# Kernel optimization log

Measured on AMD Instinct MI355X. Metric: run time of the kernel, lower is better.

Reference implementation:

```python
import jax, jax.numpy as jnp
import numpy as np

BLANK = 0
T, N, C, S = 1024, 64, 128, 128


def setup_inputs() -> dict:
    key = jax.random.key(0)
    k1, k2, k3, k4 = jax.random.split(key, 4)
    logits = jax.random.normal(k1, (T, N, C), dtype=jnp.float32)
    log_probs = jax.nn.log_softmax(logits, axis=-1)
    targets = jax.random.randint(k2, (N, S), 1, C).astype(jnp.int64)  # non-blank labels
    input_lengths = jax.random.randint(k3, (N,), T // 2, T + 1).astype(jnp.int32)
    target_lengths = jax.random.randint(k4, (N,), S // 2, S + 1).astype(jnp.int32)
    return {"log_probs": log_probs, "targets": targets,
            "input_lengths": input_lengths, "target_lengths": target_lengths}


def _ctc_loss(log_probs, targets, input_lengths, target_lengths):
    Tt, Nn, Cc = log_probs.shape
    Ss = targets.shape[1]
    Sx = 2 * Ss + 1  # extended target length (blanks interleaved)
    neg_inf = jnp.asarray(-jnp.inf, log_probs.dtype)

    ext = jnp.full((Nn, Sx), BLANK, dtype=jnp.int32).at[:, 1::2].set(targets.astype(jnp.int32))
    # emission log-prob of each extended state at each time: [T, N, Sx]
    emit = jnp.take_along_axis(log_probs, jnp.broadcast_to(ext[None], (Tt, Nn, Sx)), axis=2)
    # skip transition allowed when label[s] != label[s-2] (and s >= 2)
    skip = jnp.concatenate([jnp.zeros((Nn, 2), bool), ext[:, 2:] != ext[:, :-2]], axis=1)

    # faithful to the torch code: alphas initialized to ZEROS, then states 0,1 set
    alpha0 = jnp.zeros((Nn, Sx), log_probs.dtype)
    alpha0 = alpha0.at[:, 0].set(emit[0, :, 0]).at[:, 1].set(emit[0, :, 1])

    pad1 = jnp.full((Nn, 1), neg_inf, log_probs.dtype)
    pad2 = jnp.full((Nn, 2), neg_inf, log_probs.dtype)

    def step(alpha, emit_t):
        a_m1 = jnp.concatenate([pad1, alpha[:, :-1]], axis=1)
        a_m2 = jnp.where(skip, jnp.concatenate([pad2, alpha[:, :-2]], axis=1), neg_inf)
        new = jax.nn.logsumexp(jnp.stack([alpha, a_m1, a_m2]), axis=0) + emit_t
        return new, new

    _, rest = jax.lax.scan(step, alpha0, emit[1:])
    alphas = jnp.concatenate([alpha0[None], rest], axis=0)  # [T, N, Sx]

    n_idx = jnp.arange(Nn)
    v = alphas[input_lengths - 1, n_idx, 2 * target_lengths - 1]  # [N]
    # original: loss = -logsumexp over batch, then .mean() of a scalar (identity)
    return -jax.nn.logsumexp(v)


def reference(log_probs, targets, input_lengths, target_lengths):
    return _ctc_loss(log_probs, targets, input_lengths, target_lengths)
```

## Files before the change

### kernel.cpp

```cpp
#include <hip/hip_runtime.h>
#include <math.h>

#define TT 1024
#define NN 64
#define CC 128
#define SS 128
#define CH 32
#define NCHUNK 32
#define NC (NN * CC)

typedef float f4 __attribute__((ext_vector_type(4)));

#define DPP_QP_XOR1   0xB1
#define DPP_QP_XOR2   0x4E
#define DPP_WAVE_SHR1 0x138
#define DPP_ROW_MIRR  0x140
#define DPP_HALF_MIRR 0x141
#define DPP_BCAST15   0x142
#define DPP_BCAST31   0x143

template <int CTRL>
__device__ __forceinline__ float dpp_max_stage(float v) {
    int p = __builtin_amdgcn_update_dpp(__float_as_int(v), __float_as_int(v),
                                        CTRL, 0xF, 0xF, false);
    return fmaxf(v, __int_as_float(p));
}
__device__ __forceinline__ float dpp_shr1(float v) {
    int p = __builtin_amdgcn_update_dpp(0, __float_as_int(v),
                                        DPP_WAVE_SHR1, 0xF, 0xF, true);
    return __int_as_float(p);
}

#define DSR(dst, addr, off) \
    asm volatile("ds_read_b128 %0, %1 offset:" #off : "=v"(dst) : "v"(addr))
#define LGKM(n) do { \
    asm volatile("s_waitcnt lgkmcnt(" #n ")" ::: "memory"); \
    __builtin_amdgcn_sched_barrier(0); } while (0)
#define VMC(n) do { \
    asm volatile("s_waitcnt vmcnt(" #n ")" ::: "memory"); \
    __builtin_amdgcn_sched_barrier(0); } while (0)
#define ISSUE(mi, oea, oeb, opq) do { \
    DSR(gea[mi], base_e, oea); DSR(geb[mi], base_e, oeb); \
    DSR(gpq[mi], base_pq, opq); } while (0)
#define BARRIER() asm volatile("s_barrier" ::: "memory")

__global__ __launch_bounds__(320, 1) void ctc_scan(
    const float* __restrict__ lp,
    const int*   __restrict__ targets,
    const int*   __restrict__ ilen,
    const int*   __restrict__ tlen,
    float*       __restrict__ v_out)
{
    const int n    = blockIdx.x;
    const int tid  = threadIdx.x;
    const int wv   = tid >> 6;
    const int lane = tid & 63;

    __shared__ float  s_rows[2][CH][CC];
    __shared__ float4 s_e[2][CH / 2][64];
    __shared__ float4 s_pb4[2][CH / 4];

    const int tgA = targets[n * SS + 2 * lane];
    const int tgB = targets[n * SS + 2 * lane + 1];
    const float* lpn = lp + (size_t)n * CC;

    const int w  = wv - 1;
    const int r0 = w * 8;

    auto issue_rows = [&](int c, int buf) {
#pragma unroll
        for (int i = 0; i < 4; ++i) {
            const int r = r0 + 2 * i;
            int t = 1 + c * CH + r + (lane >> 5);
            if (t > TT - 1) t = TT - 1;
            const float* src = lpn + (size_t)t * NC + (lane & 31) * 4;
            __builtin_amdgcn_global_load_lds(
                (const __attribute__((address_space(1))) void*)src,
                (__attribute__((address_space(3))) void*)&s_rows[buf][r][0],
                16, 0, 0);
        }
    };
    auto gather = [&](int buf, int ebuf) {
#pragma unroll
        for (int i = 0; i < 4; ++i) {
            const int rA = r0 + 2 * i, rB = rA + 1;
            const float pa0 = s_rows[buf][rA][tgA], pc0 = s_rows[buf][rA][tgB];
            const float pa1 = s_rows[buf][rB][tgA], pc1 = s_rows[buf][rB][tgB];
            s_e[ebuf][(r0 >> 1) + i][lane] =
                make_float4(__expf(pa0), __expf(pc0), __expf(pa1), __expf(pc1));
        }
        if (lane < 8) {
            const float pbv = s_rows[buf][r0 + lane][0];
            ((float*)s_pb4[ebuf])[r0 + lane] = __expf(pbv);
        }
    };

    if (wv != 0) {
        issue_rows(0, 0);
        issue_rows(1, 1);
        VMC(4);
        gather(0, 0);
    }

    const int tgBm = (lane > 0) ? targets[n * SS + 2 * lane - 1] : -1;
    const float k1f = (lane > 0 && tgA != tgBm) ? 1.f : 0.f;
    const float k3f = (tgB != tgA) ? 1.f : 0.f;
    const int il    = ilen[n];
    const int vs    = 2 * tlen[n] - 1;
    const int vlane = vs >> 2;

    float a0 = 1.f, a1 = 1.f, a2 = 1.f, a3 = 1.f, ls = 0.f;
    if (wv == 0) {
        a0 = (lane == 0) ? __expf(lpn[0])   : 1.f;
        a1 = (lane == 0) ? __expf(lpn[tgA]) : 1.f;
    }
    float a3p = (lane == 0) ? 0.f : 1.f;
    float mr = 1.f, inv = 1.f;

    const unsigned base_e0  = (unsigned)(size_t)(void*)&s_e[0][0][lane];
    const unsigned base_pq0 = (unsigned)(size_t)(void*)&s_pb4[0][0];

    __syncthreads();

    for (int cc = 0; cc < NCHUNK; ++cc) {
        const int b = cc & 1;
        if (wv == 0) {
            const int t0 = 1 + cc * CH;
            const bool cap = ((unsigned)(il - 1 - t0) < (unsigned)CH);
            const unsigned base_e  = base_e0  + (unsigned)(b << 14);
            const unsigned base_pq = base_pq0 + (unsigned)(b << 7);

            f4 gea[3], geb[3], gpq[3];

            auto group4 = [&](const f4& ea, const f4& eb, const f4& pq, int jbase) {
#pragma unroll
                for (int c = 0; c < 4; ++c) {
                    const int j = jbase + c;
                    const float cpa = (c==0)?ea[0]:(c==1)?ea[2]:(c==2)?eb[0]:eb[2];
                    const float cpc = (c==0)?ea[1]:(c==1)?ea[3]:(c==2)?eb[1]:eb[3];
                    const float cpb = pq[c];

                    float nb3 = fmaf(k3f, a1, a3 + a2) * cpc;
                    float a3pn = dpp_shr1(nb3);
                    float nb0 = (a0 + a3p) * cpb;
                    float nb1 = fmaf(k1f, a3p, a0 + a1) * cpa;
                    float nb2 = (a2 + a1) * cpb;

                    const int jj = j & 7;
                    if      (jj == 0) mr = fmaxf(fmaxf(nb0, nb1), fmaxf(nb2, nb3));
                    else if (jj == 1) mr = dpp_max_stage<DPP_QP_XOR1>(mr);
                    else if (jj == 2) mr = dpp_max_stage<DPP_QP_XOR2>(mr);
                    else if (jj == 3) mr = dpp_max_stage<DPP_HALF_MIRR>(mr);
                    else if (jj == 4) mr = dpp_max_stage<DPP_ROW_MIRR>(mr);
                    else if (jj == 5) mr = dpp_max_stage<DPP_BCAST15>(mr);
                    else if (jj == 6) mr = dpp_max_stage<DPP_BCAST31>(mr);
                    else {
                        const float mru = __int_as_float(
                            __builtin_amdgcn_readlane(__float_as_int(mr), 63));
                        inv = 1.0f / mru;
                        ls += __logf(mru);
                        nb0 *= inv; nb1 *= inv; nb2 *= inv; nb3 *= inv;
                    }

                    if (cap) {
                        const int t = t0 + j;
                        if (t == il - 1 && lane == vlane)
                            v_out[n] = __logf((vs & 2) ? nb3 : nb1) + ls;
                    }

                    a0 = nb0; a1 = nb1; a2 = nb2; a3 = nb3;
                    if (jj == 7) a3pn *= inv;
                    a3p = a3pn;
                }
            };

            ISSUE(0, 0,     1024,  0);
            ISSUE(1, 2048,  3072,  16);
            ISSUE(2, 4096,  5120,  32);  LGKM(6); group4(gea[0], geb[0], gpq[0], 0);
            ISSUE(0, 6144,  7168,  48);  LGKM(6); group4(gea[1], geb[1], gpq[1], 4);
            ISSUE(1, 8192,  9216,  64);  LGKM(6); group4(gea[2], geb[2], gpq[2], 8);
            ISSUE(2, 10240, 11264, 80);  LGKM(6); group4(gea[0], geb[0], gpq[0], 12);
            ISSUE(0, 12288, 13312, 96);  LGKM(6); group4(gea[1], geb[1], gpq[1], 16);
            ISSUE(1, 14336, 15360, 112); LGKM(6); group4(gea[2], geb[2], gpq[2], 20);
                                         LGKM(3); group4(gea[0], geb[0], gpq[0], 24);
                                         LGKM(0); group4(gea[1], geb[1], gpq[1], 28);
        } else {
            issue_rows(cc + 2, cc & 1);
            VMC(4);
            if (cc + 1 < NCHUNK) gather((cc + 1) & 1, (cc + 1) & 1);
            asm volatile("s_waitcnt lgkmcnt(0)" ::: "memory");
        }
        BARRIER();
    }
}

__global__ void ctc_reduce(const float* __restrict__ v, float* __restrict__ out)
{
    const int lane = threadIdx.x;
    float x = v[lane];
    float m = x;
#pragma unroll
    for (int off = 32; off > 0; off >>= 1) m = fmaxf(m, __shfl_xor(m, off));
    float e = __expf(x - m);
#pragma unroll
    for (int off = 32; off > 0; off >>= 1) e += __shfl_xor(e, off);
    if (lane == 0) out[0] = -(m + __logf(e));
}

extern "C" void kernel_launch(void* const* d_in, const int* in_sizes, int n_in,
                              void* d_out, int out_size, void* d_ws, size_t ws_size,
                              hipStream_t stream) {
    const float* lp      = (const float*)d_in[0];
    const int*   targets = (const int*)d_in[1];
    const int*   ilen    = (const int*)d_in[2];
    const int*   tlen    = (const int*)d_in[3];

    float* v   = (float*)d_ws;
    float* out = (float*)d_out;

    ctc_scan<<<NN, 320, 0, stream>>>(lp, targets, ilen, tlen, v);
    ctc_reduce<<<1, 64, 0, stream>>>(v, out);
}
```

Before: 71.63 us.

## Fuse pairs of CTC timesteps into precomputed two-step transition coefficients

Helper waves now precompute, per pair of timesteps, a small matrix of combined emission and transition coefficients (scaled by a constant 4096 per pair). The serial scan wave then advances alpha two timesteps per step using FMAs, which halves the length of the critical dependency chain. The exact single-step path is kept only for the first chunk and for the chunk containing the input-length capture. In exchange, helper waves do more work and the pipeline uses more LDS, smaller 16-step chunks and twice as many barriers, and the fixed scale offset must be subtracted correctly in the log-scale accumulator.

```diff
diff --git a/kernel.cpp b/kernel.cpp
--- a/kernel.cpp
+++ b/kernel.cpp
@@ -5,8 +5,7 @@
 #define NN 64
 #define CC 128
 #define SS 128
-#define CH 32
-#define NCHUNK 32
+#define NCH 64
 #define NC (NN * CC)
 
 typedef float f4 __attribute__((ext_vector_type(4)));
@@ -39,10 +38,10 @@
 #define VMC(n) do { \
     asm volatile("s_waitcnt vmcnt(" #n ")" ::: "memory"); \
     __builtin_amdgcn_sched_barrier(0); } while (0)
-#define ISSUE(mi, oea, oeb, opq) do { \
-    DSR(gea[mi], base_e, oea); DSR(geb[mi], base_e, oeb); \
-    DSR(gpq[mi], base_pq, opq); } while (0)
 #define BARRIER() asm volatile("s_barrier" ::: "memory")
+#define ISSUE_C(g, bb) do { const unsigned ab = base_C + (bb) * 5120u; \
+    DSR(g##0, ab, 0); DSR(g##1, ab, 1024); DSR(g##2, ab, 2048); \
+    DSR(g##3, ab, 3072); DSR(g##4, ab, 4096); } while (0)
 
 __global__ __launch_bounds__(320, 1) void ctc_scan(
     const float* __restrict__ lp,
@@ -56,22 +55,26 @@
     const int wv   = tid >> 6;
     const int lane = tid & 63;
 
-    __shared__ float  s_rows[2][CH][CC];
-    __shared__ float4 s_e[2][CH / 2][64];
-    __shared__ float4 s_pb4[2][CH / 4];
-
-    const int tgA = targets[n * SS + 2 * lane];
-    const int tgB = targets[n * SS + 2 * lane + 1];
+    __shared__ float  s_rows[2][16][CC];
+    __shared__ f4     s_C[2][8][5][64];
+    __shared__ float4 s_e[2][8][64];
+    __shared__ float  s_pb[2][8][2];
+
+    const int tgA  = targets[n * SS + 2 * lane];
+    const int tgB  = targets[n * SS + 2 * lane + 1];
+    const int tgBm = (lane > 0) ? targets[n * SS + 2 * lane - 1] : -1;
+    const float k1f = (lane > 0 && tgA != tgBm) ? 1.f : 0.f;
+    const float k3f = (tgB != tgA) ? 1.f : 0.f;
     const float* lpn = lp + (size_t)n * CC;
 
-    const int w  = wv - 1;
-    const int r0 = w * 8;
-
-    auto issue_rows = [&](int c, int buf) {
-#pragma unroll
-        for (int i = 0; i < 4; ++i) {
-            const int r = r0 + 2 * i;
-            int t = 1 + c * CH + r + (lane >> 5);
+    const int w = wv - 1;
+    const float km1f = dpp_shr1(k3f);
+
+    auto stage_rows = [&](int c, int buf) {
+#pragma unroll
+        for (int i = 0; i < 2; ++i) {
+            const int r = 4 * w + 2 * i;
+            int t = 1 + 16 * c + r + (lane >> 5);
             if (t > TT - 1) t = TT - 1;
             const float* src = lpn + (size_t)t * NC + (lane & 31) * 4;
             __builtin_amdgcn_global_load_lds(
@@ -80,65 +83,87 @@
                 16, 0, 0);
         }
     };
-    auto gather = [&](int buf, int ebuf) {
-#pragma unroll
-        for (int i = 0; i < 4; ++i) {
-            const int rA = r0 + 2 * i, rB = rA + 1;
-            const float pa0 = s_rows[buf][rA][tgA], pc0 = s_rows[buf][rA][tgB];
-            const float pa1 = s_rows[buf][rB][tgA], pc1 = s_rows[buf][rB][tgB];
-            s_e[ebuf][(r0 >> 1) + i][lane] =
-                make_float4(__expf(pa0), __expf(pc0), __expf(pa1), __expf(pc1));
-        }
-        if (lane < 8) {
-            const float pbv = s_rows[buf][r0 + lane][0];
-            ((float*)s_pb4[ebuf])[r0 + lane] = __expf(pbv);
+
+    auto build = [&](int buf) {
+#pragma unroll
+        for (int i = 0; i < 2; ++i) {
+            const int blk = 2 * w + i;
+            const int r1 = 2 * blk, r2 = r1 + 1;
+            const float b1  = __expf(s_rows[buf][r1][0]);
+            const float x1  = __expf(s_rows[buf][r1][tgA]);
+            const float x3  = __expf(s_rows[buf][r1][tgB]);
+            const float b2r = __expf(s_rows[buf][r2][0]);
+            const float y1r = __expf(s_rows[buf][r2][tgA]);
+            const float y3r = __expf(s_rows[buf][r2][tgB]);
+            s_e[buf][blk][lane] = make_float4(x1, x3, y1r, y3r);
+            if (lane == 0) { s_pb[buf][blk][0] = b1; s_pb[buf][blk][1] = b2r; }
+
+            const float B = 4096.f;
+            const float b2 = b2r * B, y1 = y1r * B, y3 = y3r * B;
+            const float xm1 = dpp_shr1(x3);
+
+            const float C00 = b2 * b1;
+            const float C02 = b2 * xm1;
+            const float C01 = C00 + C02;
+            const float C03 = km1f * C02;
+            const float C10 = y1 * x1;
+            const float C11 = y1 * (x1 + b1);
+            const float C12 = y1 * fmaf(k1f, x1 + xm1, b1);
+            const float C13 = y1 * (k1f * xm1);
+            const float C14 = km1f * C13;
+            const float C20 = C00;
+            const float C22 = b2 * x1;
+            const float C21 = C20 + C22;
+            const float C23 = k1f * C22;
+            const float C30 = y3 * x3;
+            const float C31 = y3 * (x3 + b1);
+            const float C32 = y3 * fmaf(k3f, x3 + x1, b1);
+            const float C33 = y3 * (k3f * x1);
+            const float C34 = k1f * C33;
+
+            s_C[buf][blk][0][lane] = (f4){C00, C01, C02, C03};
+            s_C[buf][blk][1][lane] = (f4){C10, C11, C12, C13};
+            s_C[buf][blk][2][lane] = (f4){C14, C20, C21, C22};
+            s_C[buf][blk][3][lane] = (f4){C23, C30, C31, C32};
+            s_C[buf][blk][4][lane] = (f4){C33, C34, 0.f, 0.f};
         }
     };
 
-    if (wv != 0) {
-        issue_rows(0, 0);
-        issue_rows(1, 1);
-        VMC(4);
-        gather(0, 0);
-    }
-
-    const int tgBm = (lane > 0) ? targets[n * SS + 2 * lane - 1] : -1;
-    const float k1f = (lane > 0 && tgA != tgBm) ? 1.f : 0.f;
-    const float k3f = (tgB != tgA) ? 1.f : 0.f;
     const int il    = ilen[n];
     const int vs    = 2 * tlen[n] - 1;
     const int vlane = vs >> 2;
+    const int capc  = (il - 2) >> 4;
 
     float a0 = 1.f, a1 = 1.f, a2 = 1.f, a3 = 1.f, ls = 0.f;
     if (wv == 0) {
         a0 = (lane == 0) ? __expf(lpn[0])   : 1.f;
         a1 = (lane == 0) ? __expf(lpn[tgA]) : 1.f;
     }
-    float a3p = (lane == 0) ? 0.f : 1.f;
     float mr = 1.f, inv = 1.f;
 
-    const unsigned base_e0  = (unsigned)(size_t)(void*)&s_e[0][0][lane];
-    const unsigned base_pq0 = (unsigned)(size_t)(void*)&s_pb4[0][0];
-
-    __syncthreads();
-
-    for (int cc = 0; cc < NCHUNK; ++cc) {
+    const unsigned base_C0 = (unsigned)(size_t)(void*)&s_C[0][0][0][lane];
+
+    if (wv != 0) {
+        stage_rows(0, 0); stage_rows(1, 1);
+        VMC(2);
+        build(0);
+        asm volatile("s_waitcnt lgkmcnt(0)" ::: "memory");
+    }
+    BARRIER();
+
+    for (int cc = 0; cc < NCH; ++cc) {
         const int b = cc & 1;
         if (wv == 0) {
-            const int t0 = 1 + cc * CH;
-            const bool cap = ((unsigned)(il - 1 - t0) < (unsigned)CH);
-            const unsigned base_e  = base_e0  + (unsigned)(b << 14);
-            const unsigned base_pq = base_pq0 + (unsigned)(b << 7);
-
-            f4 gea[3], geb[3], gpq[3];
-
-            auto group4 = [&](const f4& ea, const f4& eb, const f4& pq, int jbase) {
-#pragma unroll
-                for (int c = 0; c < 4; ++c) {
-                    const int j = jbase + c;
-                    const float cpa = (c==0)?ea[0]:(c==1)?ea[2]:(c==2)?eb[0]:eb[2];
-                    const float cpc = (c==0)?ea[1]:(c==1)?ea[3]:(c==2)?eb[1]:eb[3];
-                    const float cpb = pq[c];
+            if (cc == 0 || cc == capc) {
+                const int t0c = 1 + 16 * cc;
+                float a3p = dpp_shr1(a3);
+#pragma unroll
+                for (int j = 0; j < 16; ++j) {
+                    const int k = j >> 1;
+                    const float4 e  = s_e[b][k][lane];
+                    const float cpb = s_pb[b][k][j & 1];
+                    const float cpa = (j & 1) ? e.z : e.x;
+                    const float cpc = (j & 1) ? e.w : e.y;
 
                     float nb3 = fmaf(k3f, a1, a3 + a2) * cpc;
                     float a3pn = dpp_shr1(nb3);
@@ -162,32 +187,69 @@
                         nb0 *= inv; nb1 *= inv; nb2 *= inv; nb3 *= inv;
                     }
 
-                    if (cap) {
-                        const int t = t0 + j;
-                        if (t == il - 1 && lane == vlane)
-                            v_out[n] = __logf((vs & 2) ? nb3 : nb1) + ls;
-                    }
+                    const int t = t0c + j;
+                    if (t == il - 1 && lane == vlane)
+                        v_out[n] = __logf((vs & 2) ? nb3 : nb1) + ls;
 
                     a0 = nb0; a1 = nb1; a2 = nb2; a3 = nb3;
                     if (jj == 7) a3pn *= inv;
                     a3p = a3pn;
                 }
-            };
-
-            ISSUE(0, 0,     1024,  0);
-            ISSUE(1, 2048,  3072,  16);
-            ISSUE(2, 4096,  5120,  32);  LGKM(6); group4(gea[0], geb[0], gpq[0], 0);
-            ISSUE(0, 6144,  7168,  48);  LGKM(6); group4(gea[1], geb[1], gpq[1], 4);
-            ISSUE(1, 8192,  9216,  64);  LGKM(6); group4(gea[2], geb[2], gpq[2], 8);
-            ISSUE(2, 10240, 11264, 80);  LGKM(6); group4(gea[0], geb[0], gpq[0], 12);
-            ISSUE(0, 12288, 13312, 96);  LGKM(6); group4(gea[1], geb[1], gpq[1], 16);
-            ISSUE(1, 14336, 15360, 112); LGKM(6); group4(gea[2], geb[2], gpq[2], 20);
-                                         LGKM(3); group4(gea[0], geb[0], gpq[0], 24);
-                                         LGKM(0); group4(gea[1], geb[1], gpq[1], 28);
+            } else {
+                const unsigned base_C = base_C0 + (unsigned)(b * 40960);
+                f4 gqA0, gqA1, gqA2, gqA3, gqA4;
+                f4 gqB0, gqB1, gqB2, gqB3, gqB4;
+                f4 gqC0, gqC1, gqC2, gqC3, gqC4;
+
+                auto bstep = [&](const f4 q0, const f4 q1, const f4 q2,
+                                 const f4 q3, const f4 q4, const int bb) {
+                    const float a1p = dpp_shr1(a1);
+                    const float a2p = dpp_shr1(a2);
+                    const float a3p = dpp_shr1(a3);
+                    float n0 = q0[0] * a0;
+                    n0 = fmaf(q0[1], a3p, n0); n0 = fmaf(q0[2], a2p, n0);
+                    n0 = fmaf(q0[3], a1p, n0);
+                    float n1 = q1[0] * a1;
+                    n1 = fmaf(q1[1], a0, n1);  n1 = fmaf(q1[2], a3p, n1);
+                    n1 = fmaf(q1[3], a2p, n1); n1 = fmaf(q2[0], a1p, n1);
+                    float n2 = q2[1] * a2;
+                    n2 = fmaf(q2[2], a1, n2);  n2 = fmaf(q2[3], a0, n2);
+                    n2 = fmaf(q3[0], a3p, n2);
+                    float n3 = q3[1] * a3;
+                    n3 = fmaf(q3[2], a2, n3);  n3 = fmaf(q3[3], a1, n3);
+                    n3 = fmaf(q4[0], a0, n3);  n3 = fmaf(q4[1], a3p, n3);
+
+                    if      (bb == 0) mr = fmaxf(fmaxf(n0, n1), fmaxf(n2, n3));
+                    else if (bb == 1) mr = dpp_max_stage<DPP_QP_XOR1>(mr);
+                    else if (bb == 2) mr = dpp_max_stage<DPP_QP_XOR2>(mr);
+                    else if (bb == 3) mr = dpp_max_stage<DPP_HALF_MIRR>(mr);
+                    else if (bb == 4) mr = dpp_max_stage<DPP_ROW_MIRR>(mr);
+                    else if (bb == 5) mr = dpp_max_stage<DPP_BCAST15>(mr);
+                    else if (bb == 6) mr = dpp_max_stage<DPP_BCAST31>(mr);
+                    else {
+                        const float mru = __int_as_float(
+                            __builtin_amdgcn_readlane(__float_as_int(mr), 63));
+                        inv = 1.0f / mru;
+                        ls += __logf(mru) - 66.542129f;
+                        n0 *= inv; n1 *= inv; n2 *= inv; n3 *= inv;
+                    }
+                    a0 = n0; a1 = n1; a2 = n2; a3 = n3;
+                };
+
+                ISSUE_C(gqA, 0); ISSUE_C(gqB, 1);
+                ISSUE_C(gqC, 2); LGKM(10); bstep(gqA0, gqA1, gqA2, gqA3, gqA4, 0);
+                ISSUE_C(gqA, 3); LGKM(10); bstep(gqB0, gqB1, gqB2, gqB3, gqB4, 1);
+                ISSUE_C(gqB, 4); LGKM(10); bstep(gqC0, gqC1, gqC2, gqC3, gqC4, 2);
+                ISSUE_C(gqC, 5); LGKM(10); bstep(gqA0, gqA1, gqA2, gqA3, gqA4, 3);
+                ISSUE_C(gqA, 6); LGKM(10); bstep(gqB0, gqB1, gqB2, gqB3, gqB4, 4);
+                ISSUE_C(gqB, 7); LGKM(10); bstep(gqC0, gqC1, gqC2, gqC3, gqC4, 5);
+                                 LGKM(5);  bstep(gqA0, gqA1, gqA2, gqA3, gqA4, 6);
+                                 LGKM(0);  bstep(gqB0, gqB1, gqB2, gqB3, gqB4, 7);
+            }
         } else {
-            issue_rows(cc + 2, cc & 1);
-            VMC(4);
-            if (cc + 1 < NCHUNK) gather((cc + 1) & 1, (cc + 1) & 1);
+            stage_rows(cc + 2, b);
+            VMC(2);
+            if (cc + 1 < NCH) build((cc + 1) & 1);
             asm volatile("s_waitcnt lgkmcnt(0)" ::: "memory");
         }
         BARRIER();
```

Result: no change. 71.89 us (+0.4%).
